# Optimization experiments

Hardware: AMD Instinct MI355X
Metric: run time of the kernel (lower is better)

## Reference

```python
import jax, jax.numpy as jnp
import numpy as np

BATCH = 2048
INPUT_DIM = 256
NUM_SUBCARRIERS = 256
HIDDEN_DIM = 256


def setup_inputs() -> dict:
    key = jax.random.key(0)
    ks = jax.random.split(key, 7)
    C, I, H = NUM_SUBCARRIERS, INPUT_DIM, HIDDEN_DIM
    # PyTorch nn.Linear default init: U(-1/sqrt(fan_in), 1/sqrt(fan_in))
    s1 = 1.0 / np.sqrt(I)
    s2 = 1.0 / np.sqrt(H)
    x = jax.random.normal(ks[0], (BATCH, I), dtype=jnp.float32)
    W1 = jax.random.uniform(ks[1], (C, I, H), jnp.float32, -s1, s1)
    b1 = jax.random.uniform(ks[2], (C, H), jnp.float32, -s1, s1)
    W2 = jax.random.uniform(ks[3], (C, H, H), jnp.float32, -s2, s2)
    b2 = jax.random.uniform(ks[4], (C, H), jnp.float32, -s2, s2)
    W3 = jax.random.uniform(ks[5], (C, H), jnp.float32, -s2, s2)  # [C, H] (out dim 1 squeezed)
    b3 = jax.random.uniform(ks[6], (C,), jnp.float32, -s2, s2)
    return {"x": x, "W1": W1, "b1": b1, "W2": W2, "b2": b2, "W3": W3, "b3": b3}


def reference(x, W1, b1, W2, b2, W3, b3):
    # Stacked (batched) version of the per-subcarrier Python loop:
    # for each subcarrier c: relu(relu(x @ W1[c] + b1[c]) @ W2[c] + b2[c]) @ W3[c] + b3[c]
    h1 = jax.nn.relu(jnp.einsum('bi,cih->cbh', x, W1) + b1[:, None, :])   # [C, B, H]
    h2 = jax.nn.relu(jnp.einsum('cbh,chk->cbk', h1, W2) + b2[:, None, :])  # [C, B, H]
    out = jnp.einsum('cbh,ch->cb', h2, W3) + b3[:, None]                   # [C, B]
    return out.T  # [B, C], matches torch.cat(outputs, dim=1)
```

## Files before the change

kernel.cpp:

```cpp
#include <hip/hip_runtime.h>

typedef unsigned short u16;
using u16x4  = __attribute__((ext_vector_type(4))) unsigned short;
using u16x8  = __attribute__((ext_vector_type(8))) unsigned short;
using bf16x8 = __attribute__((ext_vector_type(8))) short;
using f32x4  = __attribute__((ext_vector_type(4))) float;

__device__ __forceinline__ u16 f2bf(float f) {
  union { float f; unsigned u; } v; v.f = f;
  unsigned r = v.u + 0x7FFFu + ((v.u >> 16) & 1u);
  return (u16)(r >> 16);
}

__global__ void convert_x_k(const float* __restrict__ in, u16* __restrict__ out) {
  int i = blockIdx.x * 256 + threadIdx.x;
  float4 v = ((const float4*)in)[i];
  u16x4 u;
  u.x = f2bf(v.x); u.y = f2bf(v.y); u.z = f2bf(v.z); u.w = f2bf(v.w);
  ((u16x4*)out)[i] = u;
}

__global__ __launch_bounds__(256) void transpose_w2_k(
    const float* __restrict__ W1, const float* __restrict__ W2,
    u16* __restrict__ w1t, u16* __restrict__ w2t) {
  __shared__ float tile[64][65];
  const int bid = blockIdx.x;
  const int mat = bid >> 4;
  const int tl  = bid & 15;
  const int i0 = (tl >> 2) * 64, h0 = (tl & 3) * 64;
  const float* src = (mat < 256) ? (W1 + mat * 65536) : (W2 + (mat - 256) * 65536);
  u16*       dst   = (mat < 256) ? (w1t + mat * 65536) : (w2t + (mat - 256) * 65536);
  const int t = threadIdx.x;
#pragma unroll
  for (int j = 0; j < 4; ++j) {
    int lin = j * 256 + t;
    int row = lin >> 4, c4 = lin & 15;
    float4 v = *(const float4*)(src + (i0 + row) * 256 + h0 + c4 * 4);
    tile[row][c4 * 4 + 0] = v.x; tile[row][c4 * 4 + 1] = v.y;
    tile[row][c4 * 4 + 2] = v.z; tile[row][c4 * 4 + 3] = v.w;
  }
  __syncthreads();
  const int col = t >> 2;
  const int kk  = (t & 3) * 8;
#pragma unroll
  for (int p = 0; p < 2; ++p) {
    u16x8 o;
#pragma unroll
    for (int jj = 0; jj < 8; ++jj)
      o[jj] = f2bf(tile[p * 32 + kk + jj][col]);
    *(u16x8*)(dst + ((i0 >> 5) + p) * 8192 + (h0 + col) * 32 + kk) = o;
  }
}

__global__ __launch_bounds__(512, 4) void rf_main_k(
    const u16* __restrict__ xb, const u16* __restrict__ w1t, const u16* __restrict__ w2t,
    const float* __restrict__ b1, const float* __restrict__ b2,
    const float* __restrict__ w3, const float* __restrict__ b3,
    float* __restrict__ out) {
  __shared__ u16 sH[128 * 264];
  __shared__ float red[512];

  const int bid  = blockIdx.x;
  const int xcd  = bid & 7;
  const int j8   = bid >> 3;
  const int c    = xcd * 32 + (j8 >> 4);
  const int b0   = (j8 & 15) * 128;
  const int t    = threadIdx.x;
  const int lane = t & 63;
  const int w    = t >> 6;
  const int l15  = lane & 15;
  const int quad = lane >> 4;
  const int half = w >> 2;
  const int nw   = (w & 3) * 64;

  const u16* w1c = w1t + c * 65536;
  const u16* w2c = w2t + c * 65536;
  const int boff  = (nw + l15) * 32 + quad * 8;
  const int abase = (half * 64 + l15) * 264 + quad * 8;

  f32x4  acc[4][4] = {};
  bf16x8 bA[4], bB[4];

#define LOADB(dst, base)                                        \
  { _Pragma("unroll")                                           \
    for (int _n = 0; _n < 4; ++_n)                              \
      dst[_n] = *(const bf16x8*)((base) + _n * 512); }

#define COMPUTE(bfr, ch)                                        \
  { _Pragma("unroll")                                           \
    for (int _m = 0; _m < 4; ++_m) {                            \
      bf16x8 _a = *(const bf16x8*)&sH[abase + _m * (16*264) + (ch) * 32]; \
      _Pragma("unroll")                                         \
      for (int _n = 0; _n < 4; ++_n)                            \
        acc[_m][_n] = __builtin_amdgcn_mfma_f32_16x16x32_bf16(_a, bfr[_n], acc[_m][_n], 0, 0, 0); \
    } }

  LOADB(bA, w1c + boff);

#pragma unroll
  for (int i = 0; i < 8; ++i) {
    int flat = i * 512 + t;
    int r = flat >> 5, s = flat & 31;
    u16x8 g = *(const u16x8*)(xb + (b0 + r) * 256 + s * 8);
    *(u16x8*)&sH[r * 264 + s * 8] = g;
  }
  __syncthreads();

#pragma unroll 1
  for (int ch = 0; ch < 8; ch += 2) {
    LOADB(bB, w1c + (ch + 1) * 8192 + boff);
    COMPUTE(bA, ch);
    const u16* nxt = (ch == 6) ? (w2c + boff)
                               : (w1c + (ch + 2) * 8192 + boff);
    LOADB(bA, nxt);
    COMPUTE(bB, ch + 1);
  }

  __syncthreads();
#pragma unroll
  for (int ni = 0; ni < 4; ++ni) {
    int col = nw + ni * 16 + l15;
    float bias = b1[c * 256 + col];
#pragma unroll
    for (int mi = 0; mi < 4; ++mi)
#pragma unroll
      for (int r = 0; r < 4; ++r) {
        int row = half * 64 + mi * 16 + quad * 4 + r;
        float v = acc[mi][ni][r] + bias;
        v = v > 0.f ? v : 0.f;
        sH[row * 264 + col] = f2bf(v);
        acc[mi][ni][r] = 0.f;
      }
  }
  __syncthreads();

#pragma unroll 1
  for (int ch = 0; ch < 8; ch += 2) {
    LOADB(bB, w2c + (ch + 1) * 8192 + boff);
    COMPUTE(bA, ch);
    if (ch < 6) LOADB(bA, w2c + (ch + 2) * 8192 + boff);
    COMPUTE(bB, ch + 1);
  }

  float part[16];
#pragma unroll
  for (int i = 0; i < 16; ++i) part[i] = 0.f;
#pragma unroll
  for (int ni = 0; ni < 4; ++ni) {
    int col = nw + ni * 16 + l15;
    float bias = b2[c * 256 + col];
    float w3v  = w3[c * 256 + col];
#pragma unroll
    for (int mi = 0; mi < 4; ++mi)
#pragma unroll
      for (int r = 0; r < 4; ++r) {
        float v = acc[mi][ni][r] + bias;
        v = v > 0.f ? v : 0.f;
        part[mi * 4 + r] += v * w3v;
      }
  }
#pragma unroll
  for (int m = 1; m < 16; m <<= 1)
#pragma unroll
    for (int i = 0; i < 16; ++i)
      part[i] += __shfl_xor(part[i], m, 64);

  if (l15 == 0) {
#pragma unroll
    for (int mi = 0; mi < 4; ++mi)
#pragma unroll
      for (int r = 0; r < 4; ++r)
        red[w * 64 + mi * 16 + quad * 4 + r] = part[mi * 4 + r];
  }
  __syncthreads();
  if (t < 128) {
    int hr = t >> 6, rr = t & 63;
    float v = red[(hr * 4 + 0) * 64 + rr] + red[(hr * 4 + 1) * 64 + rr] +
              red[(hr * 4 + 2) * 64 + rr] + red[(hr * 4 + 3) * 64 + rr] + b3[c];
    out[(b0 + t) * 256 + c] = v;
  }
#undef LOADB
#undef COMPUTE
}

extern "C" void kernel_launch(void* const* d_in, const int* in_sizes, int n_in,
                              void* d_out, int out_size, void* d_ws, size_t ws_size,
                              hipStream_t stream) {
  const float* x  = (const float*)d_in[0];
  const float* W1 = (const float*)d_in[1];
  const float* b1 = (const float*)d_in[2];
  const float* W2 = (const float*)d_in[3];
  const float* b2 = (const float*)d_in[4];
  const float* W3 = (const float*)d_in[5];
  const float* b3 = (const float*)d_in[6];
  float* out = (float*)d_out;

  char* ws = (char*)d_ws;
  u16* xb  = (u16*)ws;
  u16* w1t = (u16*)(ws + (1u << 20));
  u16* w2t = (u16*)(ws + (1u << 20) + (32u << 20));

  convert_x_k   <<<512,  256, 0, stream>>>(x,  xb);
  transpose_w2_k<<<8192, 256, 0, stream>>>(W1, W2, w1t, w2t);
  rf_main_k     <<<4096, 512, 0, stream>>>(xb, w1t, w2t, b1, b2, W3, b3, out);
}
```

Baseline: 315.3 us.

## Switch to 32x32x16 MFMA with fragment-ordered layouts and direct-from-global layer-1 A

Replaces the 16x16x32 bf16 MFMA tiling with 32x32x16 MFMA (2x2 tiles of 32x32 per wave) and reorders the pre-converted x and transposed W1/W2 buffers so each lane's 8-element fragment is one contiguous 16-byte load. Layer 1 now streams A fragments for x straight from global memory instead of first staging x in LDS, which removes the initial LDS fill and its barrier. Layer 2 still reads the hidden activations from LDS. The larger MFMA shape does fewer instructions per FLOP and needs fewer B loads, at the cost of more global traffic for x and different register pressure.

```diff
diff --git a/kernel.cpp b/kernel.cpp
--- a/kernel.cpp
+++ b/kernel.cpp
@@ -1,10 +1,9 @@
 #include <hip/hip_runtime.h>
 
 typedef unsigned short u16;
-using u16x4  = __attribute__((ext_vector_type(4))) unsigned short;
 using u16x8  = __attribute__((ext_vector_type(8))) unsigned short;
 using bf16x8 = __attribute__((ext_vector_type(8))) short;
-using f32x4  = __attribute__((ext_vector_type(4))) float;
+using f32x16 = __attribute__((ext_vector_type(16))) float;
 
 __device__ __forceinline__ u16 f2bf(float f) {
   union { float f; unsigned u; } v; v.f = f;
@@ -12,12 +11,16 @@
   return (u16)(r >> 16);
 }
 
-__global__ void convert_x_k(const float* __restrict__ in, u16* __restrict__ out) {
-  int i = blockIdx.x * 256 + threadIdx.x;
-  float4 v = ((const float4*)in)[i];
-  u16x4 u;
-  u.x = f2bf(v.x); u.y = f2bf(v.y); u.z = f2bf(v.z); u.w = f2bf(v.w);
-  ((u16x4*)out)[i] = u;
+__global__ void convert_xA_k(const float* __restrict__ in, u16* __restrict__ out) {
+  int flat = blockIdx.x * 256 + threadIdx.x;
+  int b   = flat >> 5;
+  int oct = flat & 31;
+  const float4* src = (const float4*)(in + b * 256 + oct * 8);
+  float4 v0 = src[0], v1 = src[1];
+  u16x8 o;
+  o[0] = f2bf(v0.x); o[1] = f2bf(v0.y); o[2] = f2bf(v0.z); o[3] = f2bf(v0.w);
+  o[4] = f2bf(v1.x); o[5] = f2bf(v1.y); o[6] = f2bf(v1.z); o[7] = f2bf(v1.w);
+  *(u16x8*)(out + ((b >> 5) << 13) + ((oct >> 1) << 9) + ((b & 31) << 4) + ((oct & 1) << 3)) = o;
 }
 
 __global__ __launch_bounds__(256) void transpose_w2_k(
@@ -40,24 +43,25 @@
     tile[row][c4 * 4 + 2] = v.z; tile[row][c4 * 4 + 3] = v.w;
   }
   __syncthreads();
-  const int col = t >> 2;
-  const int kk  = (t & 3) * 8;
 #pragma unroll
   for (int p = 0; p < 2; ++p) {
+    int lin  = p * 256 + t;
+    int nloc = lin >> 3;
+    int oct  = lin & 7;
     u16x8 o;
 #pragma unroll
     for (int jj = 0; jj < 8; ++jj)
-      o[jj] = f2bf(tile[p * 32 + kk + jj][col]);
-    *(u16x8*)(dst + ((i0 >> 5) + p) * 8192 + (h0 + col) * 32 + kk) = o;
+      o[jj] = f2bf(tile[oct * 8 + jj][nloc]);
+    *(u16x8*)(dst + ((i0 >> 4) + (oct >> 1)) * 4096 + (h0 + nloc) * 16 + (oct & 1) * 8) = o;
   }
 }
 
 __global__ __launch_bounds__(512, 4) void rf_main_k(
-    const u16* __restrict__ xb, const u16* __restrict__ w1t, const u16* __restrict__ w2t,
+    const u16* __restrict__ xA, const u16* __restrict__ w1t, const u16* __restrict__ w2t,
     const float* __restrict__ b1, const float* __restrict__ b2,
     const float* __restrict__ w3, const float* __restrict__ b3,
     float* __restrict__ out) {
-  __shared__ u16 sH[128 * 264];
+  __shared__ u16 sH1[128 * 264];
   __shared__ float red[512];
 
   const int bid  = blockIdx.x;
@@ -68,119 +72,131 @@
   const int t    = threadIdx.x;
   const int lane = t & 63;
   const int w    = t >> 6;
-  const int l15  = lane & 15;
-  const int quad = lane >> 4;
+  const int l31  = lane & 31;
+  const int hi   = lane >> 5;
   const int half = w >> 2;
-  const int nw   = (w & 3) * 64;
+  const int cb   = (w & 3) * 64;
 
   const u16* w1c = w1t + c * 65536;
   const u16* w2c = w2t + c * 65536;
-  const int boff  = (nw + l15) * 32 + quad * 8;
-  const int abase = (half * 64 + l15) * 264 + quad * 8;
-
-  f32x4  acc[4][4] = {};
-  bf16x8 bA[4], bB[4];
-
-#define LOADB(dst, base)                                        \
-  { _Pragma("unroll")                                           \
-    for (int _n = 0; _n < 4; ++_n)                              \
-      dst[_n] = *(const bf16x8*)((base) + _n * 512); }
-
-#define COMPUTE(bfr, ch)                                        \
-  { _Pragma("unroll")                                           \
-    for (int _m = 0; _m < 4; ++_m) {                            \
-      bf16x8 _a = *(const bf16x8*)&sH[abase + _m * (16*264) + (ch) * 32]; \
-      _Pragma("unroll")                                         \
-      for (int _n = 0; _n < 4; ++_n)                            \
-        acc[_m][_n] = __builtin_amdgcn_mfma_f32_16x16x32_bf16(_a, bfr[_n], acc[_m][_n], 0, 0, 0); \
-    } }
-
-  LOADB(bA, w1c + boff);
-
-#pragma unroll
-  for (int i = 0; i < 8; ++i) {
-    int flat = i * 512 + t;
-    int r = flat >> 5, s = flat & 31;
-    u16x8 g = *(const u16x8*)(xb + (b0 + r) * 256 + s * 8);
-    *(u16x8*)&sH[r * 264 + s * 8] = g;
+  const int bBase = (cb + l31) * 16 + hi * 8;
+  const int aBase = ((b0 >> 5) + half * 2) * 8192 + l31 * 16 + hi * 8;
+  const int aLds  = (half * 64 + l31) * 264 + hi * 8;
+
+  f32x16 acc[2][2] = {};
+  bf16x8 a0[2], a1[2], bb0[2], bb1[2];
+
+#define LOADA(dst, s)                                             \
+  { _Pragma("unroll")                                             \
+    for (int _m = 0; _m < 2; ++_m)                                \
+      dst[_m] = *(const bf16x8*)(xA + aBase + _m * 8192 + (s) * 512); }
+#define LOADB(dst, wc, s)                                         \
+  { _Pragma("unroll")                                             \
+    for (int _n = 0; _n < 2; ++_n)                                \
+      dst[_n] = *(const bf16x8*)((wc) + bBase + _n * 512 + (s) * 4096); }
+#define COMP_G(AA, BB)                                            \
+  { _Pragma("unroll")                                             \
+    for (int _m = 0; _m < 2; ++_m)                                \
+      _Pragma("unroll")                                           \
+      for (int _n = 0; _n < 2; ++_n)                              \
+        acc[_m][_n] = __builtin_amdgcn_mfma_f32_32x32x16_bf16(AA[_m], BB[_n], acc[_m][_n], 0, 0, 0); }
+#define COMP_L(BB, s)                                             \
+  { bf16x8 _a[2];                                                 \
+    _Pragma("unroll")                                             \
+    for (int _m = 0; _m < 2; ++_m)                                \
+      _a[_m] = *(const bf16x8*)&sH1[aLds + _m * (32 * 264) + (s) * 16]; \
+    _Pragma("unroll")                                             \
+    for (int _m = 0; _m < 2; ++_m)                                \
+      _Pragma("unroll")                                           \
+      for (int _n = 0; _n < 2; ++_n)                              \
+        acc[_m][_n] = __builtin_amdgcn_mfma_f32_32x32x16_bf16(_a[_m], BB[_n], acc[_m][_n], 0, 0, 0); }
+
+  LOADA(a0, 0); LOADB(bb0, w1c, 0);
+#pragma unroll 1
+  for (int s = 0; s < 14; s += 2) {
+    LOADA(a1, s + 1); LOADB(bb1, w1c, s + 1);
+    COMP_G(a0, bb0);
+    LOADA(a0, s + 2); LOADB(bb0, w1c, s + 2);
+    COMP_G(a1, bb1);
+  }
+  LOADA(a1, 15); LOADB(bb1, w1c, 15);
+  COMP_G(a0, bb0);
+  LOADB(bb0, w2c, 0);
+  COMP_G(a1, bb1);
+
+#pragma unroll
+  for (int nt = 0; nt < 2; ++nt) {
+    int col = cb + nt * 32 + l31;
+    float bias = b1[c * 256 + col];
+#pragma unroll
+    for (int mt = 0; mt < 2; ++mt)
+#pragma unroll
+      for (int r = 0; r < 16; ++r) {
+        int row = half * 64 + mt * 32 + (r & 3) + 8 * (r >> 2) + 4 * hi;
+        float v = acc[mt][nt][r] + bias;
+        v = v > 0.f ? v : 0.f;
+        sH1[row * 264 + col] = f2bf(v);
+        acc[mt][nt][r] = 0.f;
+      }
   }
   __syncthreads();
 
 #pragma unroll 1
-  for (int ch = 0; ch < 8; ch += 2) {
-    LOADB(bB, w1c + (ch + 1) * 8192 + boff);
-    COMPUTE(bA, ch);
-    const u16* nxt = (ch == 6) ? (w2c + boff)
-                               : (w1c + (ch + 2) * 8192 + boff);
-    LOADB(bA, nxt);
-    COMPUTE(bB, ch + 1);
-  }
-
-  __syncthreads();
-#pragma unroll
-  for (int ni = 0; ni < 4; ++ni) {
-    int col = nw + ni * 16 + l15;
-    float bias = b1[c * 256 + col];
-#pragma unroll
-    for (int mi = 0; mi < 4; ++mi)
-#pragma unroll
-      for (int r = 0; r < 4; ++r) {
-        int row = half * 64 + mi * 16 + quad * 4 + r;
-        float v = acc[mi][ni][r] + bias;
-        v = v > 0.f ? v : 0.f;
-        sH[row * 264 + col] = f2bf(v);
-        acc[mi][ni][r] = 0.f;
-      }
-  }
-  __syncthreads();
-
-#pragma unroll 1
-  for (int ch = 0; ch < 8; ch += 2) {
-    LOADB(bB, w2c + (ch + 1) * 8192 + boff);
-    COMPUTE(bA, ch);
-    if (ch < 6) LOADB(bA, w2c + (ch + 2) * 8192 + boff);
-    COMPUTE(bB, ch + 1);
-  }
-
-  float part[16];
-#pragma unroll
-  for (int i = 0; i < 16; ++i) part[i] = 0.f;
-#pragma unroll
-  for (int ni = 0; ni < 4; ++ni) {
-    int col = nw + ni * 16 + l15;
+  for (int s = 0; s < 14; s += 2) {
+    LOADB(bb1, w2c, s + 1);
+    COMP_L(bb0, s);
+    LOADB(bb0, w2c, s + 2);
+    COMP_L(bb1, s + 1);
+  }
+  LOADB(bb1, w2c, 15);
+  COMP_L(bb0, 14);
+  COMP_L(bb1, 15);
+
+  float part[2][16];
+#pragma unroll
+  for (int mt = 0; mt < 2; ++mt)
+#pragma unroll
+    for (int r = 0; r < 16; ++r) part[mt][r] = 0.f;
+#pragma unroll
+  for (int nt = 0; nt < 2; ++nt) {
+    int col = cb + nt * 32 + l31;
     float bias = b2[c * 256 + col];
     float w3v  = w3[c * 256 + col];
 #pragma unroll
-    for (int mi = 0; mi < 4; ++mi)
-#pragma unroll
-      for (int r = 0; r < 4; ++r) {
-        float v = acc[mi][ni][r] + bias;
+    for (int mt = 0; mt < 2; ++mt)
+#pragma unroll
+      for (int r = 0; r < 16; ++r) {
+        float v = acc[mt][nt][r] + bias;
         v = v > 0.f ? v : 0.f;
-        part[mi * 4 + r] += v * w3v;
+        part[mt][r] += v * w3v;
       }
   }
 #pragma unroll
-  for (int m = 1; m < 16; m <<= 1)
-#pragma unroll
-    for (int i = 0; i < 16; ++i)
-      part[i] += __shfl_xor(part[i], m, 64);
-
-  if (l15 == 0) {
-#pragma unroll
-    for (int mi = 0; mi < 4; ++mi)
-#pragma unroll
-      for (int r = 0; r < 4; ++r)
-        red[w * 64 + mi * 16 + quad * 4 + r] = part[mi * 4 + r];
+  for (int m = 1; m < 32; m <<= 1)
+#pragma unroll
+    for (int mt = 0; mt < 2; ++mt)
+#pragma unroll
+      for (int r = 0; r < 16; ++r)
+        part[mt][r] += __shfl_xor(part[mt][r], m, 64);
+
+  if (l31 == 0) {
+#pragma unroll
+    for (int mt = 0; mt < 2; ++mt)
+#pragma unroll
+      for (int r = 0; r < 16; ++r) {
+        int row = half * 64 + mt * 32 + (r & 3) + 8 * (r >> 2) + 4 * hi;
+        red[(w & 3) * 128 + row] = part[mt][r];
+      }
   }
   __syncthreads();
   if (t < 128) {
-    int hr = t >> 6, rr = t & 63;
-    float v = red[(hr * 4 + 0) * 64 + rr] + red[(hr * 4 + 1) * 64 + rr] +
-              red[(hr * 4 + 2) * 64 + rr] + red[(hr * 4 + 3) * 64 + rr] + b3[c];
+    float v = red[t] + red[128 + t] + red[256 + t] + red[384 + t] + b3[c];
     out[(b0 + t) * 256 + c] = v;
   }
+#undef LOADA
 #undef LOADB
-#undef COMPUTE
+#undef COMP_G
+#undef COMP_L
 }
 
 extern "C" void kernel_launch(void* const* d_in, const int* in_sizes, int n_in,
@@ -196,11 +212,11 @@
   float* out = (float*)d_out;
 
   char* ws = (char*)d_ws;
-  u16* xb  = (u16*)ws;
+  u16* xA  = (u16*)ws;
   u16* w1t = (u16*)(ws + (1u << 20));
   u16* w2t = (u16*)(ws + (1u << 20) + (32u << 20));
 
-  convert_x_k   <<<512,  256, 0, stream>>>(x,  xb);
+  convert_xA_k  <<<256,  256, 0, stream>>>(x,  xA);
   transpose_w2_k<<<8192, 256, 0, stream>>>(W1, W2, w1t, w2t);
-  rf_main_k     <<<4096, 512, 0, stream>>>(xb, w1t, w2t, b1, b2, W3, b3, out);
-}
+  rf_main_k     <<<4096, 512, 0, stream>>>(xA, w1t, w2t, b1, b2, W3, b3, out);
+}
```

Result: slower. 326.7 us (+3.6%).
